# Performance work log

Measured on AMD Instinct MI355X. Metric: run time of the kernel, lower is better.

The kernel has to match this reference:

```python
import jax, jax.numpy as jnp
import numpy as np

# ---- static dims (from init_kwargs / Hydra defaults) ----
B_, N_MESH, G, HEADS, DH = 2, 100000, 64, 8, 64
DIM = 256
D_MODEL = HEADS * DH              # 512
EXPAND, D_STATE, D_CONV = 2, 64, 3
D_INNER = EXPAND * D_MODEL        # 1024
HEADDIM = 64
NHEADS = D_INNER // HEADDIM       # 16
CONV_DIM = D_INNER + 2 * D_STATE  # 1152
D_IN_PROJ = 2 * D_INNER + 2 * D_STATE + 2 * NHEADS  # 2208


def _ssd_scan(x, dt, A, B, C):
    """Selective state-space scan (SSD / Mamba2 recurrence).
    x:(bb,L,H,P) dt:(bb,L,H) A:(H,) B,C:(bb,L,N). Returns y:(bb,L,H,P)."""
    bb, L, H, P = x.shape
    N = B.shape[-1]
    xs = jnp.moveaxis(x, 1, 0)   # (L,bb,H,P)
    dts = jnp.moveaxis(dt, 1, 0)  # (L,bb,H)
    Bs = jnp.moveaxis(B, 1, 0)   # (L,bb,N)
    Cs = jnp.moveaxis(C, 1, 0)
    h0 = jnp.zeros((bb, H, P, N), x.dtype)

    def step(h, inp):
        x_t, dt_t, B_t, C_t = inp
        dA = jnp.exp(dt_t * A)                                   # (bb,H)
        h = dA[..., None, None] * h + (dt_t[..., None] * x_t)[..., None] * B_t[:, None, None, :]
        y_t = jnp.einsum('bhpn,bn->bhp', h, C_t)
        return h, y_t

    _, ys = jax.lax.scan(step, h0, (xs, dts, Bs, Cs))
    return jnp.moveaxis(ys, 0, 1)


def _hydra(u, in_proj_w, conv_w, conv_b, dt_bias, A_log, fc_D_w, D, norm_w, out_proj_w):
    """Hydra (bidirectional Mamba2) forward, slow (non mem-eff) path."""
    b, L, _ = u.shape
    zxbcdt = u @ in_proj_w.T                                     # (b,L,2208)
    z = zxbcdt[..., :D_INNER]
    xBC = zxbcdt[..., D_INNER:D_INNER + CONV_DIM]
    dt_raw = zxbcdt[..., D_INNER + CONV_DIM:]                    # (b,L,2*NHEADS)
    # forward heads + time-flipped backward heads stacked along batch
    dt = jnp.concatenate([dt_raw[..., :NHEADS], jnp.flip(dt_raw[..., NHEADS:], axis=1)], axis=0)
    dt = jax.nn.softplus(dt + dt_bias)                           # (2b,L,NHEADS)
    # depthwise non-causal 'same' conv1d + SiLU
    xBC = jax.lax.conv_general_dilated(
        xBC.transpose(0, 2, 1), conv_w, (1,), [(1, 1)],
        dimension_numbers=('NCH', 'OIH', 'NCH'), feature_group_count=CONV_DIM)
    xBC = jax.nn.silu(xBC + conv_b[None, :, None]).transpose(0, 2, 1)
    x = xBC[..., :D_INNER]
    Bc = xBC[..., D_INNER:D_INNER + D_STATE]
    Cc = xBC[..., D_INNER + D_STATE:]
    x_og = x
    x2 = jnp.concatenate([x, jnp.flip(x, 1)], 0).reshape(2 * b, L, NHEADS, HEADDIM)
    B2 = jnp.concatenate([Bc, jnp.flip(Bc, 1)], 0)
    C2 = jnp.concatenate([Cc, jnp.flip(Cc, 1)], 0)
    A = -jnp.exp(A_log)                                          # (NHEADS,)
    y = _ssd_scan(x2, dt, A, B2, C2).reshape(2 * b, L, D_INNER)
    # shift by one (strictly off-diagonal parts), zero first position
    y = jnp.pad(y[:, :-1], ((0, 0), (1, 0), (0, 0)))
    diag = x_og @ fc_D_w.T + D                                   # (b,L,NHEADS)
    y = y[:b] + jnp.flip(y[b:], 1) + x_og * jnp.repeat(diag, HEADDIM, axis=-1)
    # gated RMSNorm
    y = y * jax.nn.silu(z)
    y = y * jax.lax.rsqrt(jnp.mean(y * y, axis=-1, keepdims=True) + 1e-5) * norm_w
    return y @ out_proj_w.T                                      # (b,L,D_MODEL)


def _forward(slice_token, slice_weights, in_proj_w, conv_w, conv_b, dt_bias, A_log,
             fc_D_w, D, norm_w, out_proj_w, to_out_w, to_out_b):
    b, h, g, c = slice_token.shape
    u = slice_token.transpose(0, 2, 1, 3).reshape(b, g, h * c)   # b g (h c)
    out = _hydra(u, in_proj_w, conv_w, conv_b, dt_bias, A_log, fc_D_w, D, norm_w, out_proj_w)
    ost = out.reshape(b, g, h, c).transpose(0, 2, 1, 3)          # b h g c
    out_x = jnp.einsum('bhgc,bhng->bhnc', ost, slice_weights)    # gather back to mesh points
    out_x = out_x.transpose(0, 2, 1, 3).reshape(b, out_x.shape[2], h * c)  # b n (h c)
    return out_x @ to_out_w.T + to_out_b


def setup_inputs() -> dict:
    key = jax.random.key(0)
    ks = jax.random.split(key, 14)
    f32 = jnp.float32
    inp = {}
    inp['slice_token'] = jax.random.normal(ks[0], (B_, HEADS, G, DH), f32)
    inp['slice_weights'] = jax.random.uniform(ks[1], (B_, HEADS, N_MESH, G), f32)
    inp['in_proj_w'] = jax.random.normal(ks[2], (D_IN_PROJ, D_MODEL), f32) * (D_MODEL ** -0.5)
    inp['conv_w'] = jax.random.normal(ks[3], (CONV_DIM, 1, D_CONV), f32) * 0.3
    inp['conv_b'] = jax.random.normal(ks[4], (CONV_DIM,), f32) * 0.02
    inp['dt_bias'] = jnp.log(jnp.expm1(jax.random.uniform(ks[5], (NHEADS,), f32, 0.001, 0.1)))
    inp['A_log'] = jnp.log(jax.random.uniform(ks[6], (NHEADS,), f32, 1.0, 8.0))
    inp['fc_D_w'] = jax.random.normal(ks[7], (NHEADS, D_INNER), f32) * (D_INNER ** -0.5)
    inp['D'] = jax.random.normal(ks[8], (NHEADS,), f32) * 0.1 + 1.0
    inp['norm_w'] = jnp.ones((D_INNER,), f32)
    inp['out_proj_w'] = jax.random.normal(ks[9], (D_MODEL, D_INNER), f32) * (D_INNER ** -0.5)
    inp['to_out_w'] = jax.random.normal(ks[10], (DIM, D_MODEL), f32) * (D_MODEL ** -0.5)
    inp['to_out_b'] = jnp.zeros((DIM,), f32)
    return inp


def reference(slice_token, slice_weights, in_proj_w, conv_w, conv_b, dt_bias, A_log,
              fc_D_w, D, norm_w, out_proj_w, to_out_w, to_out_b):
    return _forward(slice_token, slice_weights, in_proj_w, conv_w, conv_b, dt_bias,
                    A_log, fc_D_w, D, norm_w, out_proj_w, to_out_w, to_out_b)
```

## Files before the change

### kernel.cpp

```cpp
#include <hip/hip_runtime.h>
#include <hip/hip_bf16.h>
#include <math.h>

#define NB 2
#define LL 64
#define NMESH 100000
#define HEADS_O 8
#define DHC 64
#define DMODEL 512
#define DINNER 1024
#define DSTATE 64
#define NH 16
#define CONVDIM 1152
#define DINPROJ 2208
#define DOUT 256
#define NCHUNK 6250

typedef __attribute__((ext_vector_type(8))) short short8v;
typedef __attribute__((ext_vector_type(4))) float f32x4;

__device__ __forceinline__ unsigned short f2bf(float f) {
  union { float f; unsigned u; } v; v.f = f;
  unsigned u = v.u;
  u += 0x7FFFu + ((u >> 16) & 1u);
  return (unsigned short)(u >> 16);
}

__device__ __forceinline__ float dot4(float4 a, const float* b) {
  return a.x*b[0] + a.y*b[1] + a.z*b[2] + a.w*b[3];
}

__device__ __forceinline__ float silu(float s) { return s / (1.f + expf(-s)); }

#define GLDS(g, l) __builtin_amdgcn_global_load_lds( \
    (const __attribute__((address_space(1))) void*)(g), \
    (__attribute__((address_space(3))) void*)(l), 16, 0, 0)

__global__ void k_inproj(const float* __restrict__ st, const float* __restrict__ w,
                         float* __restrict__ zx) {
  int oc = blockIdx.x;
  int blc = blockIdx.y;
  int t = threadIdx.x;
  __shared__ float u[8][DMODEL];
  for (int idx = t; idx < 8*DMODEL; idx += 256) {
    int r = idx >> 9, m = idx & 511;
    int bl = blc*8 + r; int b = bl >> 6, l = bl & 63;
    u[r][m] = st[((size_t)(b*HEADS_O + (m >> 6))*LL + l)*DHC + (m & 63)];
  }
  __syncthreads();
  int o = oc*256 + t;
  if (o < DINPROJ) {
    const float4* wr = (const float4*)(w + (size_t)o*DMODEL);
    float acc[8] = {0,0,0,0,0,0,0,0};
    for (int m4 = 0; m4 < DMODEL/4; ++m4) {
      float4 wv = wr[m4];
      #pragma unroll
      for (int r = 0; r < 8; ++r) acc[r] += dot4(wv, &u[r][m4*4]);
    }
    #pragma unroll
    for (int r = 0; r < 8; ++r)
      zx[(size_t)(blc*8 + r)*DINPROJ + o] = acc[r];
  }
}

__global__ void k_convdt(const float* __restrict__ zx, const float* __restrict__ cw,
                         const float* __restrict__ cb, const float* __restrict__ dtb,
                         float* __restrict__ conv_out, float* __restrict__ dtbuf) {
  if (blockIdx.x < 576) {
    int i = blockIdx.x*256 + threadIdx.x;
    int c = i % CONVDIM; int l = (i / CONVDIM) % LL; int b = i / (CONVDIM*LL);
    float s = cb[c];
    #pragma unroll
    for (int k = 0; k < 3; ++k) {
      int tt = l - 1 + k;
      if (tt >= 0 && tt < LL)
        s += cw[c*3 + k] * zx[(size_t)(b*LL + tt)*DINPROJ + DINNER + c];
    }
    conv_out[i] = silu(s);
  } else {
    int i = (blockIdx.x - 576)*256 + threadIdx.x;
    if (i < 4*LL*NH) {
      int h = i & 15, l = (i >> 4) & 63, s = i >> 10;
      float v;
      if (s < 2)
        v = zx[(size_t)(s*LL + l)*DINPROJ + (DINNER + CONVDIM) + h];
      else
        v = zx[(size_t)((s-2)*LL + (63-l))*DINPROJ + (DINNER + CONVDIM) + 16 + h];
      v += dtb[h];
      dtbuf[i] = (v > 20.f) ? v : log1pf(expf(v));
    }
  }
}

__global__ void k_scan(const float* __restrict__ conv_out, const float* __restrict__ dtbuf,
                       const float* __restrict__ A_log, float* __restrict__ ybuf) {
  int blk = blockIdx.x;
  int s = blk >> 4, hh = blk & 15;
  int b = s & 1;
  bool rev = (s >= 2);
  int t = threadIdx.x;
  int wv = t >> 6, lane = t & 63;
  __shared__ float Bs[64*68];
  __shared__ float Cs[64*68];
  __shared__ float Xs[64*64];
  __shared__ float dts[64];
  __shared__ float Dc[64];

  for (int id = t; id < 4096; id += 256) {
    int tt0 = id >> 6, n = id & 63;
    int tt = rev ? (63 - tt0) : tt0;
    size_t base = (size_t)(b*LL + tt) * CONVDIM;
    Xs[tt0*64 + n] = conv_out[base + hh*64 + n];
    Bs[tt0*68 + n] = conv_out[base + DINNER + n];
    Cs[tt0*68 + n] = conv_out[base + DINNER + DSTATE + n];
  }
  if (t < 64) dts[t] = dtbuf[(size_t)(s*LL + t)*NH + hh];
  __syncthreads();
  if (t < 64) {
    float v = dts[t];
    #pragma unroll
    for (int m = 1; m < 64; m <<= 1) {
      float o = __shfl_up(v, m, 64);
      if (lane >= m) v += o;
    }
    Dc[t] = v;
  }
  __syncthreads();
  float A = -expf(A_log[hh]);
  float g[16];
  #pragma unroll
  for (int i = 0; i < 16; ++i) {
    int tt = wv + 4*i;
    int ta = lane;
    float gv = 0.f;
    if (ta <= tt) {
      const float* Br = &Bs[ta*68];
      const float* Cr = &Cs[tt*68];
      float dot = 0.f;
      #pragma unroll
      for (int n4 = 0; n4 < 16; ++n4) {
        float4 bv = *(const float4*)&Br[n4*4];
        float4 cv = *(const float4*)&Cr[n4*4];
        dot += bv.x*cv.x + bv.y*cv.y + bv.z*cv.z + bv.w*cv.w;
      }
      gv = dot * expf(A * (Dc[tt] - Dc[ta])) * dts[ta];
    }
    g[i] = gv;
  }
  __syncthreads();
  #pragma unroll
  for (int i = 0; i < 16; ++i) Bs[(wv + 4*i)*64 + lane] = g[i];
  __syncthreads();
  for (int id = t; id < 4096; id += 256) {
    int tt = id >> 6, p = id & 63;
    float y = 0.f;
    for (int ta = 0; ta <= tt; ++ta) y += Bs[tt*64 + ta] * Xs[ta*64 + p];
    ybuf[(size_t)(s*LL + tt)*DINNER + hh*64 + p] = y;
  }
}

__global__ void k_norm(const float* __restrict__ conv_out, const float* __restrict__ zx,
                       const float* __restrict__ yb, const float* __restrict__ fcD,
                       const float* __restrict__ Dd, const float* __restrict__ nw,
                       float* __restrict__ ynorm) {
  int bl = blockIdx.x; int b = bl >> 6, l = bl & 63;
  int t = threadIdx.x;
  __shared__ float xog[DINNER];
  __shared__ float diag[NH];
  __shared__ float wsum[4];
  size_t base = (size_t)bl * CONVDIM;
  for (int c = t; c < DINNER; c += 256) xog[c] = conv_out[base + c];
  __syncthreads();
  {
    int hh = t >> 4, j = t & 15;
    const float* fr = fcD + (size_t)hh*DINNER;
    float acc = 0.f;
    for (int k = 0; k < 64; ++k) acc += xog[j + 16*k] * fr[j + 16*k];
    #pragma unroll
    for (int m = 8; m >= 1; m >>= 1) acc += __shfl_xor(acc, m, 64);
    if (j == 0) diag[hh] = acc + Dd[hh];
  }
  __syncthreads();
  float ss = 0.f;
  float y2v[4];
  #pragma unroll
  for (int i = 0; i < 4; ++i) {
    int c = t + 256*i;
    float yf = (l == 0)  ? 0.f : yb[(size_t)(b*LL + l - 1)*DINNER + c];
    float yw = (l == 63) ? 0.f : yb[(size_t)((2+b)*LL + 62 - l)*DINNER + c];
    float y1 = yf + yw + xog[c]*diag[c >> 6];
    float z = zx[(size_t)bl*DINPROJ + c];
    float y2 = y1 * silu(z);
    y2v[i] = y2;
    ss += y2*y2;
  }
  #pragma unroll
  for (int m = 32; m >= 1; m >>= 1) ss += __shfl_xor(ss, m, 64);
  if ((t & 63) == 0) wsum[t >> 6] = ss;
  __syncthreads();
  float tot = wsum[0] + wsum[1] + wsum[2] + wsum[3];
  float scale = rsqrtf(tot * (1.f/1024.f) + 1e-5f);
  #pragma unroll
  for (int i = 0; i < 4; ++i) {
    int c = t + 256*i;
    ynorm[(size_t)bl*DINNER + c] = y2v[i] * scale * nw[c];
  }
}

__global__ void k_oproj(const float* __restrict__ ynorm, const float* __restrict__ opw,
                        float* __restrict__ oh) {
  int oc = blockIdx.x;
  int blc = blockIdx.y;
  int t = threadIdx.x;
  __shared__ float yr[4][DINNER];
  for (int idx = t; idx < 4*DINNER; idx += 256) {
    int r = idx >> 10, k = idx & 1023;
    yr[r][k] = ynorm[(size_t)(blc*4 + r)*DINNER + k];
  }
  __syncthreads();
  int o = oc*256 + t;
  const float4* wr = (const float4*)(opw + (size_t)o*DINNER);
  float acc[4] = {0,0,0,0};
  for (int k4 = 0; k4 < DINNER/4; ++k4) {
    float4 wv = wr[k4];
    #pragma unroll
    for (int r = 0; r < 4; ++r) acc[r] += dot4(wv, &yr[r][k4*4]);
  }
  #pragma unroll
  for (int r = 0; r < 4; ++r)
    oh[(size_t)(blc*4 + r)*DMODEL + o] = acc[r];
}

__global__ void k_mfrag(const float* __restrict__ oh, const float* __restrict__ tow,
                        unsigned short* __restrict__ mfp) {
  int bgc = blockIdx.x;
  int dc  = blockIdx.y;
  int t = threadIdx.x;
  __shared__ float orow[8][DMODEL];
  for (int idx = t; idx < 8*DMODEL; idx += 256) {
    int r = idx >> 9, m = idx & 511;
    orow[r][m] = oh[(size_t)(bgc*8 + r)*DMODEL + m];
  }
  __syncthreads();
  #pragma unroll
  for (int ii = 0; ii < 2; ++ii) {
    int idx = t + 256*ii;
    int h = idx >> 6, dl = idx & 63;
    int d = dc*64 + dl;
    const float4* wr = (const float4*)(tow + (size_t)d*DMODEL + h*64);
    float acc[8] = {0,0,0,0,0,0,0,0};
    #pragma unroll
    for (int c4 = 0; c4 < 16; ++c4) {
      float4 wv = wr[c4];
      #pragma unroll
      for (int r = 0; r < 8; ++r) acc[r] += dot4(wv, &orow[r][h*64 + c4*4]);
    }
    #pragma unroll
    for (int r = 0; r < 8; ++r) {
      int bg = bgc*8 + r; int b = bg >> 6, g = bg & 63;
      int kk = g >> 5;
      int ln = (d & 15) | (((g & 31) >> 3) << 4);
      int j = g & 7;
      mfp[((((size_t)(b*HEADS_O + h)*2 + kk)*16 + (d >> 4))*64 + ln)*8 + j] = f2bf(acc[r]);
    }
  }
}

__global__ __launch_bounds__(512, 2) void k_out_gemm(const float* __restrict__ W,
                                                     const unsigned short* __restrict__ mf,
                                                     const float* __restrict__ tob,
                                                     float* __restrict__ out) {
  int bx = blockIdx.x;
  int b    = bx >> 7;
  int base = bx & 127;
  int tid = threadIdx.x;
  int wv = tid >> 6, lane = tid & 63;
  int r16 = lane & 15, kg = lane >> 4;

  __shared__ __align__(16) float lsA[2][16][512];

  short8v B0[16], B1[16];
  {
    const unsigned short* mfb = mf + (size_t)b*(16*16*512) + lane*8;
    #pragma unroll
    for (int ks = 0; ks < 16; ++ks) {
      B0[ks] = *(const short8v*)(mfb + ((size_t)ks*16 + 2*wv    )*512);
      B1[ks] = *(const short8v*)(mfb + ((size_t)ks*16 + 2*wv + 1)*512);
    }
  }
  float bias0 = tob[wv*32 + r16];
  float bias1 = tob[wv*32 + 16 + r16];

  #define STAGE(cc, p) do { \
    _Pragma("unroll") \
    for (int q = 0; q < 2; ++q) { \
      int ksl = 2*wv + q; \
      int h = ksl >> 1, kk = ksl & 1; \
      const float* src = W + ((size_t)(b*HEADS_O + h)*NMESH + (size_t)(cc)*16 + r16)*64 \
                           + kk*32 + kg*8; \
      GLDS(src,     &lsA[p][ksl][0]);   \
      GLDS(src + 4, &lsA[p][ksl][256]); \
    } \
  } while (0)

  int c = base;
  int p = 0;
  STAGE(c, 0);
  asm volatile("s_waitcnt vmcnt(0)" ::: "memory");
  __builtin_amdgcn_s_barrier();
  __builtin_amdgcn_sched_barrier(0);

  while (true) {
    int cn = c + 128;
    bool more = (cn < NCHUNK);
    if (more) STAGE(cn, p ^ 1);

    f32x4 acc0 = (f32x4){0.f,0.f,0.f,0.f};
    f32x4 acc1 = (f32x4){0.f,0.f,0.f,0.f};
    #pragma unroll
    for (int ks = 0; ks < 16; ++ks) {
      const float* as = &lsA[p][ks][0];
      float4 a0 = *(const float4*)(as + lane*4);
      float4 a1 = *(const float4*)(as + 256 + lane*4);
      short8v af;
      af[0] = (short)f2bf(a0.x); af[1] = (short)f2bf(a0.y);
      af[2] = (short)f2bf(a0.z); af[3] = (short)f2bf(a0.w);
      af[4] = (short)f2bf(a1.x); af[5] = (short)f2bf(a1.y);
      af[6] = (short)f2bf(a1.z); af[7] = (short)f2bf(a1.w);
      acc0 = __builtin_amdgcn_mfma_f32_16x16x32_bf16(af, B0[ks], acc0, 0, 0, 0);
      acc1 = __builtin_amdgcn_mfma_f32_16x16x32_bf16(af, B1[ks], acc1, 0, 0, 0);
    }

    int rb = c*16 + kg*4;
    int cg = wv*32 + r16;
    #pragma unroll
    for (int r = 0; r < 4; ++r) {
      out[((size_t)b*NMESH + rb + r)*DOUT + cg]      = acc0[r] + bias0;
      out[((size_t)b*NMESH + rb + r)*DOUT + cg + 16] = acc1[r] + bias1;
    }

    if (!more) break;
    asm volatile("s_waitcnt vmcnt(8) lgkmcnt(0)" ::: "memory");
    __builtin_amdgcn_s_barrier();
    __builtin_amdgcn_sched_barrier(0);
    p ^= 1;
    c = cn;
  }
  #undef STAGE
}

extern "C" void kernel_launch(void* const* d_in, const int* in_sizes, int n_in,
                              void* d_out, int out_size, void* d_ws, size_t ws_size,
                              hipStream_t stream) {
  (void)in_sizes; (void)n_in; (void)out_size; (void)ws_size;
  const float* st   = (const float*)d_in[0];
  const float* sw   = (const float*)d_in[1];
  const float* ipw  = (const float*)d_in[2];
  const float* cw   = (const float*)d_in[3];
  const float* cb   = (const float*)d_in[4];
  const float* dtb  = (const float*)d_in[5];
  const float* alog = (const float*)d_in[6];
  const float* fcD  = (const float*)d_in[7];
  const float* Dd   = (const float*)d_in[8];
  const float* nw   = (const float*)d_in[9];
  const float* opw  = (const float*)d_in[10];
  const float* tow  = (const float*)d_in[11];
  const float* tob  = (const float*)d_in[12];
  float* out = (float*)d_out;
  unsigned char* ws = (unsigned char*)d_ws;

  float* zx   = (float*)(ws + 0);
  float* conv = (float*)(ws + 1130496);
  float* dtp  = (float*)(ws + 1720320);
  float* yb   = (float*)(ws + 1736704);
  float* ynm  = (float*)(ws + 2785280);
  float* oh   = (float*)(ws + 3309568);
  unsigned short* mfr = (unsigned short*)(ws + 3571712);

  k_inproj  <<<dim3(9, 16), 256, 0, stream>>>(st, ipw, zx);
  k_convdt  <<<592, 256, 0, stream>>>(zx, cw, cb, dtb, conv, dtp);
  k_scan    <<<64,  256, 0, stream>>>(conv, dtp, alog, yb);
  k_norm    <<<128, 256, 0, stream>>>(conv, zx, yb, fcD, Dd, nw, ynm);
  k_oproj   <<<dim3(2, 32), 256, 0, stream>>>(ynm, opw, oh);
  k_mfrag   <<<dim3(16, 4), 256, 0, stream>>>(oh, tow, mfr);
  k_out_gemm<<<256, 512, 0, stream>>>(sw, mfr, tob, out);
}
```

Baseline: 295.1 us.

## Convert A tiles to bf16 once in registers before staging to LDS

The output GEMM kernel now loads each fp32 A-tile slice into registers with plain global loads, packs it to bf16 per wave, and writes it to a bf16 LDS buffer. This replaces the direct global-to-LDS fp32 copies that all waves then read back and converted redundantly. Each wave now converts its A slice once instead of every wave converting all 16 k-slices, and LDS footprint and read traffic are halved. In exchange it adds register staging, and launch bounds drop to one block per SIMD-pair hint, which may reduce occupancy and latency hiding.

```diff
diff --git a/kernel.cpp b/kernel.cpp
--- a/kernel.cpp
+++ b/kernel.cpp
@@ -26,15 +26,20 @@
   return (unsigned short)(u >> 16);
 }
 
+__device__ __forceinline__ short8v pack_bf16(float4 lo, float4 hi) {
+  short8v r;
+  r[0] = (short)f2bf(lo.x); r[1] = (short)f2bf(lo.y);
+  r[2] = (short)f2bf(lo.z); r[3] = (short)f2bf(lo.w);
+  r[4] = (short)f2bf(hi.x); r[5] = (short)f2bf(hi.y);
+  r[6] = (short)f2bf(hi.z); r[7] = (short)f2bf(hi.w);
+  return r;
+}
+
 __device__ __forceinline__ float dot4(float4 a, const float* b) {
   return a.x*b[0] + a.y*b[1] + a.z*b[2] + a.w*b[3];
 }
 
 __device__ __forceinline__ float silu(float s) { return s / (1.f + expf(-s)); }
-
-#define GLDS(g, l) __builtin_amdgcn_global_load_lds( \
-    (const __attribute__((address_space(1))) void*)(g), \
-    (__attribute__((address_space(3))) void*)(l), 16, 0, 0)
 
 __global__ void k_inproj(const float* __restrict__ st, const float* __restrict__ w,
                          float* __restrict__ zx) {
@@ -266,7 +271,7 @@
   }
 }
 
-__global__ __launch_bounds__(512, 2) void k_out_gemm(const float* __restrict__ W,
+__global__ __launch_bounds__(512, 1) void k_out_gemm(const float* __restrict__ W,
                                                      const unsigned short* __restrict__ mf,
                                                      const float* __restrict__ tob,
                                                      float* __restrict__ out) {
@@ -277,7 +282,7 @@
   int wv = tid >> 6, lane = tid & 63;
   int r16 = lane & 15, kg = lane >> 4;
 
-  __shared__ __align__(16) float lsA[2][16][512];
+  __shared__ __align__(16) unsigned short lsA[2][16][512];
 
   short8v B0[16], B1[16];
   {
@@ -291,42 +296,39 @@
   float bias0 = tob[wv*32 + r16];
   float bias1 = tob[wv*32 + 16 + r16];
 
-  #define STAGE(cc, p) do { \
-    _Pragma("unroll") \
-    for (int q = 0; q < 2; ++q) { \
-      int ksl = 2*wv + q; \
-      int h = ksl >> 1, kk = ksl & 1; \
-      const float* src = W + ((size_t)(b*HEADS_O + h)*NMESH + (size_t)(cc)*16 + r16)*64 \
-                           + kk*32 + kg*8; \
-      GLDS(src,     &lsA[p][ksl][0]);   \
-      GLDS(src + 4, &lsA[p][ksl][256]); \
-    } \
+  const float* wbase = W + ((size_t)(b*HEADS_O + wv)*NMESH + r16)*64 + kg*8;
+
+  float4 s00, s01, s10, s11;
+  #define ALOAD(cc) do { \
+    const float* p0 = wbase + (size_t)(cc)*1024; \
+    s00 = *(const float4*)p0;        s01 = *(const float4*)(p0 + 4); \
+    s10 = *(const float4*)(p0 + 32); s11 = *(const float4*)(p0 + 36); \
   } while (0)
+  #define AWRITE(pp) do { \
+    *(short8v*)&lsA[pp][2*wv    ][lane*8] = pack_bf16(s00, s01); \
+    *(short8v*)&lsA[pp][2*wv + 1][lane*8] = pack_bf16(s10, s11); \
+  } while (0)
+
+  ALOAD(base);
+  AWRITE(0);
+  asm volatile("s_waitcnt lgkmcnt(0)" ::: "memory");
+  __builtin_amdgcn_sched_barrier(0);
+  __builtin_amdgcn_s_barrier();
+  __builtin_amdgcn_sched_barrier(0);
 
   int c = base;
   int p = 0;
-  STAGE(c, 0);
-  asm volatile("s_waitcnt vmcnt(0)" ::: "memory");
-  __builtin_amdgcn_s_barrier();
-  __builtin_amdgcn_sched_barrier(0);
-
-  while (true) {
+  for (;;) {
     int cn = c + 128;
     bool more = (cn < NCHUNK);
-    if (more) STAGE(cn, p ^ 1);
+    if (more) ALOAD(cn);
+    __builtin_amdgcn_sched_barrier(0);
 
     f32x4 acc0 = (f32x4){0.f,0.f,0.f,0.f};
     f32x4 acc1 = (f32x4){0.f,0.f,0.f,0.f};
     #pragma unroll
     for (int ks = 0; ks < 16; ++ks) {
-      const float* as = &lsA[p][ks][0];
-      float4 a0 = *(const float4*)(as + lane*4);
-      float4 a1 = *(const float4*)(as + 256 + lane*4);
-      short8v af;
-      af[0] = (short)f2bf(a0.x); af[1] = (short)f2bf(a0.y);
-      af[2] = (short)f2bf(a0.z); af[3] = (short)f2bf(a0.w);
-      af[4] = (short)f2bf(a1.x); af[5] = (short)f2bf(a1.y);
-      af[6] = (short)f2bf(a1.z); af[7] = (short)f2bf(a1.w);
+      short8v af = *(const short8v*)&lsA[p][ks][lane*8];
       acc0 = __builtin_amdgcn_mfma_f32_16x16x32_bf16(af, B0[ks], acc0, 0, 0, 0);
       acc1 = __builtin_amdgcn_mfma_f32_16x16x32_bf16(af, B1[ks], acc1, 0, 0, 0);
     }
@@ -340,13 +342,17 @@
     }
 
     if (!more) break;
-    asm volatile("s_waitcnt vmcnt(8) lgkmcnt(0)" ::: "memory");
+    __builtin_amdgcn_sched_barrier(0);
+    AWRITE(p ^ 1);
+    asm volatile("s_waitcnt lgkmcnt(0)" ::: "memory");
+    __builtin_amdgcn_sched_barrier(0);
     __builtin_amdgcn_s_barrier();
     __builtin_amdgcn_sched_barrier(0);
     p ^= 1;
     c = cn;
   }
-  #undef STAGE
+  #undef ALOAD
+  #undef AWRITE
 }
 
 extern "C" void kernel_launch(void* const* d_in, const int* in_sizes, int n_in,
```

After: 241.9 us. 18.0% less time.
